# Kernel optimization log

Measured on AMD Instinct MI355X. Metric: run time of the kernel, lower is better.

## Reference

```python
import jax, jax.numpy as jnp
import numpy as np

G, A = 1024, 20          # graphs, atoms per graph
N = G * A                # nodes = 20480
E = G * A * A            # fc edges within each graph = 409600
H = 128                  # hidden_dim
LATENT = 256             # latent_dim
L = 4                    # num_layers
NFREQ = 10
DIS_DIM = NFREQ * 2 * 3  # 60
EDGE_IN = 2 * H + 9 + DIS_DIM  # 325
MAX_ATOMS = 100


def _lin(k, fin, fout):
    return jax.random.normal(k, (fin, fout), dtype=jnp.float32) / np.sqrt(fin).astype(np.float32)


def _stack_lin(k, fin, fout):
    return jnp.stack([_lin(jax.random.fold_in(k, i), fin, fout) for i in range(L)])


def setup_inputs() -> dict:
    key = jax.random.key(0)
    ks = jax.random.split(key, 16)
    atom_types = jax.random.randint(ks[0], (N,), 0, MAX_ATOMS, dtype=jnp.int32)
    frac_coords = jax.random.uniform(ks[1], (N, 3), dtype=jnp.float32)
    lattices = jax.random.normal(ks[2], (G, 3, 3), dtype=jnp.float32)
    t = jax.random.normal(ks[3], (G, LATENT), dtype=jnp.float32)
    # fully-connected (fc) edges within each graph, block-diagonal structure
    base = np.arange(A)
    src = np.repeat(base, A)
    dst = np.tile(base, A)
    offs = (np.arange(G) * A)[:, None]
    edge_index = jnp.asarray(np.stack([
        (src[None, :] + offs).reshape(-1),
        (dst[None, :] + offs).reshape(-1)]), dtype=jnp.int32)  # [2, E]
    edge2graph = jnp.asarray(np.repeat(np.arange(G), A * A), dtype=jnp.int32)
    node2graph = jnp.asarray(np.repeat(np.arange(G), A), dtype=jnp.int32)
    # parameters
    emb_table = jax.random.normal(ks[4], (MAX_ATOMS, H), dtype=jnp.float32) * 0.02
    w_latent = _lin(ks[5], H + LATENT, H)
    b_latent = jnp.zeros((H,), jnp.float32)
    edge_w1 = _stack_lin(ks[6], EDGE_IN, H)
    edge_b1 = jnp.zeros((L, H), jnp.float32)
    edge_w2 = _stack_lin(ks[7], H, H)
    edge_b2 = jnp.zeros((L, H), jnp.float32)
    node_w1 = _stack_lin(ks[8], 2 * H, H)
    node_b1 = jnp.zeros((L, H), jnp.float32)
    node_w2 = _stack_lin(ks[9], H, H)
    node_b2 = jnp.zeros((L, H), jnp.float32)
    coord_w = _lin(ks[10], H, 3)
    lattice_w = _lin(ks[11], H, 9)
    return dict(atom_types=atom_types, frac_coords=frac_coords, lattices=lattices, t=t,
                edge_index=edge_index, edge2graph=edge2graph, node2graph=node2graph,
                emb_table=emb_table, w_latent=w_latent, b_latent=b_latent,
                edge_w1=edge_w1, edge_b1=edge_b1, edge_w2=edge_w2, edge_b2=edge_b2,
                node_w1=node_w1, node_b1=node_b1, node_w2=node_w2, node_b2=node_b2,
                coord_w=coord_w, lattice_w=lattice_w)


def reference(atom_types, frac_coords, lattices, t, edge_index, edge2graph, node2graph,
              emb_table, w_latent, b_latent,
              edge_w1, edge_b1, edge_w2, edge_b2,
              node_w1, node_b1, node_w2, node_b2,
              coord_w, lattice_w):
    silu = jax.nn.silu
    src, dst = edge_index[0], edge_index[1]
    # node embedding + latent conditioning
    h = emb_table[atom_types]                               # [N,H]
    h = jnp.concatenate([h, t[node2graph]], axis=1) @ w_latent + b_latent  # [N,H]
    # sinusoidal distance embedding of periodic frac diff (detached in original)
    frac_diff = (frac_coords[dst] - frac_coords[src]) % 1.0  # [E,3]
    freqs = 2.0 * jnp.pi * jnp.arange(NFREQ, dtype=frac_coords.dtype)
    emb = (frac_diff[..., None] * freqs).reshape(-1, 3 * NFREQ)
    dis = jax.lax.stop_gradient(jnp.concatenate([jnp.sin(emb), jnp.cos(emb)], axis=-1))  # [E,60]
    # lattice inner products, broadcast to edges (ip=True)
    lat_ip = jnp.einsum('gij,gkj->gik', lattices, lattices).reshape(-1, 9)
    lat_edges = lat_ip[edge2graph]                          # [E,9]
    # per-node edge counts for scatter-mean
    counts = jax.ops.segment_sum(jnp.ones_like(src, dtype=h.dtype), src, num_segments=N)
    inv_counts = (1.0 / jnp.maximum(counts, 1.0))[:, None]
    for i in range(L):
        e_in = jnp.concatenate([h[src], h[dst], lat_edges, dis], axis=1)  # [E,325]
        ef = silu(e_in @ edge_w1[i] + edge_b1[i])
        ef = silu(ef @ edge_w2[i] + edge_b2[i])               # [E,H]
        agg = jax.ops.segment_sum(ef, src, num_segments=N) * inv_counts   # scatter-mean
        n_in = jnp.concatenate([h, agg], axis=1)              # [N,2H]
        nf = silu(n_in @ node_w1[i] + node_b1[i])
        nf = silu(nf @ node_w2[i] + node_b2[i])
        h = h + nf                                            # residual
    coord_out = h @ coord_w                                   # [N,3]
    gcounts = jax.ops.segment_sum(jnp.ones((h.shape[0],), h.dtype), node2graph, num_segments=G)
    graph_feat = jax.ops.segment_sum(h, node2graph, num_segments=G) / gcounts[:, None]
    lattice_out = (graph_feat @ lattice_w).reshape(-1, 3, 3)
    lattice_out = jnp.einsum('bij,bjk->bik', lattice_out, lattices)  # ip=True
    return lattice_out, coord_out
```

## Files before the change

kernel.cpp:

```cpp
#include <hip/hip_runtime.h>
#include <stdint.h>


#define NA 20
#define HH 128

typedef unsigned short U16;
typedef unsigned int   U32;
typedef __attribute__((ext_vector_type(8))) short bf8;
typedef __attribute__((ext_vector_type(4))) float f4;

__device__ __forceinline__ float bf2f(U16 u){ return __uint_as_float(((U32)u)<<16); }
__device__ __forceinline__ U16 f2bf(float f){
    return (U16)((__float_as_uint(f) + 0x8000u) >> 16);
}
__device__ __forceinline__ float silu_f(float x){ return x/(1.0f+__expf(-x)); }
template<bool BF>
__device__ __forceinline__ float ldf(const void* p, long i){
    return BF ? bf2f(((const U16*)p)[i]) : ((const float*)p)[i];
}
__device__ __forceinline__ f4 mfma(bf8 a, bf8 b, f4 c){
    return __builtin_amdgcn_mfma_f32_16x16x32_bf16(a,b,c,0,0,0);
}
__device__ __forceinline__ bf8 ldsA(const U16* base, int stride, int row0,
                                    int kbase, int lrow, int quad){
    return *(const bf8*)(base + (row0+lrow)*stride + kbase + quad*8);
}
template<bool BF, bool WS>
__device__ __forceinline__ bf8 getB(const U16* wsb, long wbase, int kt, int nt,
                                    int lane, const void* W, long gbase, int N,
                                    int col, int kbase, int kmax, int quad){
    if constexpr(WS){
        return *(const bf8*)(wsb + wbase + (((long)kt*8 + nt)*64 + lane)*8);
    } else {
        bf8 b; int ks0 = kbase + quad*8;
#pragma unroll
        for(int j=0;j<8;j++){
            int k=ks0+j; U16 v=0;
            if(k<kmax) v = BF ? ((const U16*)W)[gbase+(long)k*N+col]
                              : f2bf(((const float*)W)[gbase+(long)k*N+col]);
            b[j]=(short)v;
        }
        return b;
    }
}

#define WS_LBASE(L) (49152 + (long)(L)*106496)
#define REPACK_BYTES 950272

__global__ __launch_bounds__(256) void repack(
    const void* wlat, const void* ew1, const void* ew2,
    const void* nw1p, const void* nw2p, const void* lat, U16* out)
{
    __shared__ int sG[4];
    const int tid=threadIdx.x;
    {
        const U16* l16=(const U16*)lat; int good=0;
#pragma unroll
        for(int u=0;u<32;u++){
            U16 x=l16[tid*32+u]; int e=(x>>7)&0xFF; good+=(e>=100&&e<=150)?1:0;
        }
#pragma unroll
        for(int o=32;o>0;o>>=1) good+=__shfl_xor(good,o);
        if((tid&63)==0) sG[tid>>6]=good;
    }
    __syncthreads();
    const bool bf = (sG[0]+sG[1]+sG[2]+sG[3]) > 6144;

    const void* W; long srow; int segk; long dst;
    const int ktg=blockIdx.x;
    if(ktg<12){ W=wlat; srow=(long)ktg*32; segk=32; dst=(long)ktg*4096; }
    else{
        int r=ktg-12, L=r/26, lk=r-26*L;
        dst = 49152 + (long)L*106496 + (long)lk*4096;
        if(lk<4)      { W=ew1;  srow=(long)L*325+lk*32;          segk=32; }
        else if(lk<8) { W=ew1;  srow=(long)L*325+128+(lk-4)*32;  segk=32; }
        else if(lk<10){ W=ew1;  srow=(long)L*325+265+(lk-8)*32;  segk=60-(lk-8)*32; }
        else if(lk<14){ W=ew2;  srow=(long)L*128+(lk-10)*32;     segk=32; }
        else if(lk<22){ W=nw1p; srow=(long)L*256+(lk-14)*32;     segk=32; }
        else          { W=nw2p; srow=(long)L*128+(lk-22)*32;     segk=32; }
    }
    for(int o=tid;o<4096;o+=256){
        int nt=o>>9, lane=(o>>3)&63, j=o&7;
        int kk=((lane>>4)<<3)+j, col=nt*16+(lane&15);
        U16 v=0;
        if(kk<segk){
            long idx=(srow+kk)*128+col;
            v = bf ? ((const U16*)W)[idx] : f2bf(((const float*)W)[idx]);
        }
        out[dst+o]=v;
    }
}

#define PB_OFF 8960
#define QB_OFF 11520
#define DB_OFF 14080
#define EB_OFF 19840

template<bool BF, bool WS>
__device__ void body(U16* sm, float* red, const U16* wsb, int g, int tid,
    const int* __restrict__ atype, const void* frac, const void* lattices,
    const void* t, const void* emb, const void* wlat, const void* blat,
    const void* ew1, const void* eb1, const void* ew2, const void* eb2,
    const void* nw1p, const void* nb1, const void* nw2p, const void* nb2,
    const void* coordw, const void* latw, void* outv)
{
    const int lane=tid&63, w=tid>>6, lrow=lane&15, quad=lane>>4;
    const int c = w*16 + lrow;
    U16* HA=sm; U16* pB=sm+PB_OFF; U16* qB=sm+QB_OFF;
    U16* dB=sm+DB_OFF; U16* eB=sm+EB_OFF;
    U16* k1A=eB;
    float* tvecF=(float*)dB;

    for(int q=tid;q<8960;q+=512) HA[q]=0;
    for(int q=tid;q<32*136;q+=512){
        int n=q/136, cc=q-n*136; U16 v=0;
        if(n<20 && cc<128)
            v = BF ? ((const U16*)emb)[(long)atype[g*NA+n]*HH+cc]
                   : f2bf(((const float*)emb)[(long)atype[g*NA+n]*HH+cc]);
        k1A[q]=v;
    }
    {
        int sl=tid>>7, j=tid&127; float acc=0.f;
        for(int kk=0;kk<64;kk++){
            int k=sl*64+kk;
            acc += ldf<BF>(t,(long)g*256+k)*ldf<BF>(wlat,(long)(HH+k)*HH+j);
        }
        tvecF[sl*128+j]=acc;
    }
    __syncthreads();
    {
        f4 a0={0.f,0.f,0.f,0.f}, a1={0.f,0.f,0.f,0.f};
#pragma unroll
        for(int ks=0;ks<4;ks++){
            bf8 b=getB<BF,WS>(wsb,0,ks,w,lane, wlat,0,HH,c,ks*32,128,quad);
            bf8 v0=ldsA(k1A,136,0,ks*32,lrow,quad);
            bf8 v1=ldsA(k1A,136,16,ks*32,lrow,quad);
            a0=mfma(v0,b,a0); a1=mfma(v1,b,a1);
        }
        float bias=ldf<BF>(blat,c)+tvecF[c]+tvecF[128+c]+tvecF[256+c]+tvecF[384+c];
#pragma unroll
        for(int r=0;r<4;r++){
            int r0=quad*4+r, r1=16+quad*4+r;
            if(r0<20) HA[r0*280+c]=f2bf(a0[r]+bias);
            if(r1<20) HA[r1*280+c]=f2bf(a1[r]+bias);
        }
    }
    __syncthreads();
    for(int q=tid;q<80*72;q+=512) dB[q]=0;

    for(int L=0;L<4;L++){
        const long e1=(long)L*325*HH;
        const long LB=WS_LBASE(L);
        if(tid<HH){
            float la[9];
#pragma unroll
            for(int m2=0;m2<9;m2++) la[m2]=ldf<BF>(lattices,(long)g*9+m2);
            float Rv=ldf<BF>(eb1,(long)L*HH+tid);
#pragma unroll
            for(int a2=0;a2<3;a2++)
#pragma unroll
            for(int b3=0;b3<3;b3++){
                float ip=0.f;
#pragma unroll
                for(int c2=0;c2<3;c2++) ip+=la[a2*3+c2]*la[b3*3+c2];
                Rv += ip*ldf<BF>(ew1, e1+(long)(256+a2*3+b3)*HH+tid);
            }
            red[tid]=Rv;
        }
        __syncthreads();
        {
            f4 p0={0.f,0.f,0.f,0.f}, p1={0.f,0.f,0.f,0.f};
#pragma unroll
            for(int ks=0;ks<4;ks++){
                bf8 b=getB<BF,WS>(wsb,LB,ks,w,lane, ew1,e1,HH,c,ks*32,128,quad);
                bf8 v0=ldsA(HA,280,0,ks*32,lrow,quad);
                bf8 v1=ldsA(HA,280,16,ks*32,lrow,quad);
                p0=mfma(v0,b,p0); p1=mfma(v1,b,p1);
            }
            float Rc=red[c];
#pragma unroll
            for(int r=0;r<4;r++){
                int r0=quad*4+r, r1=16+quad*4+r;
                if(r0<20) pB[r0*HH+c]=f2bf(p0[r]+Rc);
                if(r1<20) pB[r1*HH+c]=f2bf(p1[r]+Rc);
            }
        }
        {
            f4 q0={0.f,0.f,0.f,0.f}, q1={0.f,0.f,0.f,0.f};
#pragma unroll
            for(int ks=0;ks<4;ks++){
                bf8 b=getB<BF,WS>(wsb,LB+16384,ks,w,lane, ew1,e1+128*HH,HH,c,ks*32,128,quad);
                bf8 v0=ldsA(HA,280,0,ks*32,lrow,quad);
                bf8 v1=ldsA(HA,280,16,ks*32,lrow,quad);
                q0=mfma(v0,b,q0); q1=mfma(v1,b,q1);
            }
#pragma unroll
            for(int r=0;r<4;r++){
                int r0=quad*4+r, r1=16+quad*4+r;
                if(r0<20) qB[r0*HH+c]=f2bf(q0[r]);
                if(r1<20) qB[r1*HH+c]=f2bf(q1[r]);
            }
        }
        bf8 w1d0=getB<BF,WS>(wsb,LB+32768,0,w,lane, ew1,e1+(long)265*HH,HH,c,0, 60,quad);
        bf8 w1d1=getB<BF,WS>(wsb,LB+32768,1,w,lane, ew1,e1+(long)265*HH,HH,c,32,60,quad);
        bf8 w2f[4];
#pragma unroll
        for(int ks=0;ks<4;ks++)
            w2f[ks]=getB<BF,WS>(wsb,LB+40960,ks,w,lane, ew2,(long)L*HH*HH,HH,c,ks*32,128,quad);
        const float b2=ldf<BF>(eb2,(long)L*HH+c);
        __syncthreads();

        for(int ch=0;ch<5;ch++){
            for(int p=tid;p<2400;p+=512){
                int r=p/30, kk=p-r*30;
                int dim=kk/10, f=kk-dim*10;
                int s=ch*4+(r&3), d=r>>2;
                float fs=ldf<BF>(frac,(long)(g*NA+s)*3+dim);
                float fd=ldf<BF>(frac,(long)(g*NA+d)*3+dim);
                float rev=(float)f*(fd-fs);
                rev=__builtin_amdgcn_fractf(rev);
                dB[r*72+kk]   =f2bf(__builtin_amdgcn_sinf(rev));
                dB[r*72+kk+30]=f2bf(__builtin_amdgcn_cosf(rev));
            }
            __syncthreads();
            float pv[4];
#pragma unroll
            for(int r=0;r<4;r++) pv[r]=bf2f(pB[(ch*4+r)*HH+c]);
#pragma unroll
            for(int m=0;m<5;m++){
                f4 a={0.f,0.f,0.f,0.f};
                bf8 v0=ldsA(dB,72,m*16,0, lrow,quad);
                bf8 v1=ldsA(dB,72,m*16,32,lrow,quad);
                a=mfma(v0,w1d0,a); a=mfma(v1,w1d1,a);
                float qd=bf2f(qB[(m*4+quad)*HH+c]);
#pragma unroll
                for(int r=0;r<4;r++){
                    int row=m*16+quad*4+r;
                    eB[row*136+c]=f2bf(silu_f(a[r]+pv[r]+qd));
                }
            }
            __syncthreads();
            float part[4]={0.f,0.f,0.f,0.f};
#pragma unroll
            for(int m=0;m<5;m++){
                f4 a={0.f,0.f,0.f,0.f};
#pragma unroll
                for(int ks=0;ks<4;ks++){
                    bf8 v=ldsA(eB,136,m*16,ks*32,lrow,quad);
                    a=mfma(v,w2f[ks],a);
                }
#pragma unroll
                for(int r=0;r<4;r++) part[r]+=silu_f(a[r]+b2);
            }
#pragma unroll
            for(int r=0;r<4;r++){
                float v=part[r];
                v+=__shfl_xor(v,16); v+=__shfl_xor(v,32);
                part[r]=v;
            }
            if(quad==0){
#pragma unroll
                for(int r=0;r<4;r++)
                    HA[(ch*4+r)*280+128+c]=f2bf(part[r]*0.05f);
            }
            __syncthreads();
        }
        {
            f4 a0={0.f,0.f,0.f,0.f}, a1={0.f,0.f,0.f,0.f};
#pragma unroll
            for(int ks=0;ks<8;ks++){
                bf8 b=getB<BF,WS>(wsb,LB+57344,ks,w,lane, nw1p,(long)L*256*HH,HH,c,ks*32,256,quad);
                bf8 v0=ldsA(HA,280,0,ks*32,lrow,quad);
                bf8 v1=ldsA(HA,280,16,ks*32,lrow,quad);
                a0=mfma(v0,b,a0); a1=mfma(v1,b,a1);
            }
            float n1=ldf<BF>(nb1,(long)L*HH+c);
#pragma unroll
            for(int r=0;r<4;r++){
                int r0=quad*4+r, r1=16+quad*4+r;
                eB[r0*136+c]=f2bf(r0<20 ? silu_f(a0[r]+n1) : 0.f);
                eB[r1*136+c]=f2bf(r1<20 ? silu_f(a1[r]+n1) : 0.f);
            }
        }
        __syncthreads();
        {
            f4 a0={0.f,0.f,0.f,0.f}, a1={0.f,0.f,0.f,0.f};
#pragma unroll
            for(int ks=0;ks<4;ks++){
                bf8 b=getB<BF,WS>(wsb,LB+90112,ks,w,lane, nw2p,(long)L*HH*HH,HH,c,ks*32,128,quad);
                bf8 v0=ldsA(eB,136,0,ks*32,lrow,quad);
                bf8 v1=ldsA(eB,136,16,ks*32,lrow,quad);
                a0=mfma(v0,b,a0); a1=mfma(v1,b,a1);
            }
            float n2=ldf<BF>(nb2,(long)L*HH+c);
#pragma unroll
            for(int r=0;r<4;r++){
                int r0=quad*4+r, r1=16+quad*4+r;
                if(r0<20) HA[r0*280+c]=f2bf(bf2f(HA[r0*280+c])+silu_f(a0[r]+n2));
                if(r1<20) HA[r1*280+c]=f2bf(bf2f(HA[r1*280+c])+silu_f(a1[r]+n2));
            }
        }
        __syncthreads();
    }

    if(tid<60){
        int n=tid/3, cc=tid-(tid/3)*3; float acc=0.f;
        for(int k=0;k<HH;k++) acc+=bf2f(HA[n*280+k])*ldf<BF>(coordw,(long)k*3+cc);
        if(BF) ((U16*)outv)[(long)1024*9+(long)(g*NA+n)*3+cc]=f2bf(acc);
        else   ((float*)outv)[(long)1024*9+(long)(g*NA+n)*3+cc]=acc;
    }
    if(tid<HH){
        float s2=0.f;
        for(int n=0;n<NA;n++) s2+=bf2f(HA[n*280+tid]);
        red[tid]=s2*0.05f;
    }
    __syncthreads();
    if(tid<9){
        float acc=0.f;
        for(int k=0;k<HH;k++) acc+=red[k]*ldf<BF>(latw,(long)k*9+tid);
        red[HH+tid]=acc;
    }
    __syncthreads();
    if(tid<9){
        int i2=tid/3, k2=tid-(tid/3)*3; float acc=0.f;
#pragma unroll
        for(int j3=0;j3<3;j3++)
            acc+=red[HH+i2*3+j3]*ldf<BF>(lattices,(long)g*9+j3*3+k2);
        if(BF) ((U16*)outv)[(long)g*9+tid]=f2bf(acc);
        else   ((float*)outv)[(long)g*9+tid]=acc;
    }
}

template<bool WS>
__device__ void mega_impl(const U16* wsb,
    const int* atype, const void* frac, const void* lattices, const void* t,
    const void* emb, const void* wlat, const void* blat,
    const void* ew1, const void* eb1, const void* ew2, const void* eb2,
    const void* nw1p, const void* nb1, const void* nw2p, const void* nb2,
    const void* coordw, const void* latw, void* outv)
{
    __shared__ __align__(16) unsigned char smraw[62080];
    U16* sm = (U16*)smraw;
    float* red = (float*)(smraw+61440);
    const int g=blockIdx.x, tid=threadIdx.x, w=tid>>6, lane=tid&63;
    int* di=(int*)red;
    {
        const U16* l16=(const U16*)lattices; int good=0;
#pragma unroll
        for(int u=0;u<16;u++){
            U16 x=l16[tid*16+u]; int e=(x>>7)&0xFF; good+=(e>=100&&e<=150)?1:0;
        }
#pragma unroll
        for(int o=32;o>0;o>>=1) good+=__shfl_xor(good,o);
        if(lane==0) di[w]=good;
    }
    __syncthreads();
    if(tid==0){ int s=0; for(int i=0;i<8;i++) s+=di[i]; di[8]=(s>6144)?1:0; }
    __syncthreads();
    const int bfm=di[8];
    __syncthreads();
    if(bfm) body<true ,WS>(sm,red,wsb,g,tid,atype,frac,lattices,t,emb,wlat,blat,
                           ew1,eb1,ew2,eb2,nw1p,nb1,nw2p,nb2,coordw,latw,outv);
    else    body<false,WS>(sm,red,wsb,g,tid,atype,frac,lattices,t,emb,wlat,blat,
                           ew1,eb1,ew2,eb2,nw1p,nb1,nw2p,nb2,coordw,latw,outv);
}

__global__ __launch_bounds__(512,2) void mega_ws(const U16* wsb,
    const int* atype, const void* frac, const void* lattices, const void* t,
    const void* emb, const void* wlat, const void* blat,
    const void* ew1, const void* eb1, const void* ew2, const void* eb2,
    const void* nw1p, const void* nb1, const void* nw2p, const void* nb2,
    const void* coordw, const void* latw, void* outv)
{
    mega_impl<true>(wsb,atype,frac,lattices,t,emb,wlat,blat,ew1,eb1,ew2,eb2,
                    nw1p,nb1,nw2p,nb2,coordw,latw,outv);
}

__global__ __launch_bounds__(512,2) void mega_direct(const U16* wsb,
    const int* atype, const void* frac, const void* lattices, const void* t,
    const void* emb, const void* wlat, const void* blat,
    const void* ew1, const void* eb1, const void* ew2, const void* eb2,
    const void* nw1p, const void* nb1, const void* nw2p, const void* nb2,
    const void* coordw, const void* latw, void* outv)
{
    mega_impl<false>(wsb,atype,frac,lattices,t,emb,wlat,blat,ew1,eb1,ew2,eb2,
                     nw1p,nb1,nw2p,nb2,coordw,latw,outv);
}

extern "C" void kernel_launch(void* const* d_in, const int* in_sizes, int n_in,
                              void* d_out, int out_size, void* d_ws, size_t ws_size,
                              hipStream_t stream)
{
    (void)in_sizes; (void)n_in; (void)out_size;
    const int* atype = (const int*)d_in[0];
    if(ws_size >= REPACK_BYTES){
        repack<<<116, 256, 0, stream>>>(d_in[8], d_in[10], d_in[12], d_in[14],
                                        d_in[16], d_in[2], (U16*)d_ws);
        mega_ws<<<1024, 512, 0, stream>>>((const U16*)d_ws,
            atype, d_in[1], d_in[2], d_in[3], d_in[7], d_in[8], d_in[9],
            d_in[10], d_in[11], d_in[12], d_in[13], d_in[14], d_in[15],
            d_in[16], d_in[17], d_in[18], d_in[19], d_out);
    } else {
        mega_direct<<<1024, 512, 0, stream>>>(nullptr,
            atype, d_in[1], d_in[2], d_in[3], d_in[7], d_in[8], d_in[9],
            d_in[10], d_in[11], d_in[12], d_in[13], d_in[14], d_in[15],
            d_in[16], d_in[17], d_in[18], d_in[19], d_out);
    }
}
```

Baseline: 437.5 us.

## Precompute per-node sin/cos tables and build edge distance features via angle-difference identities

Per-node sin/cos of f*frac are computed once into a shared table. Edge distance features then come from the sin/cos angle-difference identities instead of transcendentals per edge. Staging of the next chunk's features is moved after the barrier, so one barrier per chunk is removed. The final coord and lattice projections are spread across more threads with shuffle reductions. This adds about 4.8KB of LDS, which could affect occupancy at 2 blocks per CU, and the identity may change rounding slightly versus fract-then-sin.

```diff
diff --git a/kernel.cpp b/kernel.cpp
--- a/kernel.cpp
+++ b/kernel.cpp
@@ -97,8 +97,24 @@
 #define DB_OFF 14080
 #define EB_OFF 19840
 
+__device__ __forceinline__ void stage_dis(U16* dB, const float* tb, int ch, int tid){
+    const float2* t2=(const float2*)tb;
+#pragma unroll
+    for(int it=0; it<5; ++it){
+        int p = tid + it*512;
+        int r = p>>5, j = p&31;
+        if(j<30){
+            int s = ch*4 + (r&3), d = r>>2;
+            float2 vs = t2[s*30+j];
+            float2 vd = t2[d*30+j];
+            dB[r*72+j]    = f2bf(vd.x*vs.y - vd.y*vs.x);
+            dB[r*72+j+30] = f2bf(vd.y*vs.y + vd.x*vs.x);
+        }
+    }
+}
+
 template<bool BF, bool WS>
-__device__ void body(U16* sm, float* red, const U16* wsb, int g, int tid,
+__device__ void body(U16* sm, float* red, float* tb, const U16* wsb, int g, int tid,
     const int* __restrict__ atype, const void* frac, const void* lattices,
     const void* t, const void* emb, const void* wlat, const void* blat,
     const void* ew1, const void* eb1, const void* ew2, const void* eb2,
@@ -120,6 +136,16 @@
                    : f2bf(((const float*)emb)[(long)atype[g*NA+n]*HH+cc]);
         k1A[q]=v;
     }
+    for(int q=tid;q<600;q+=512){
+        int n=q/30, jj=q-n*30;
+        int dim=jj/10, f=jj-dim*10;
+        float x = ldf<BF>(frac,(long)(g*NA+n)*3+dim);
+        float rev = __builtin_amdgcn_fractf((float)f*x);
+        float2 sc;
+        sc.x=__builtin_amdgcn_sinf(rev);
+        sc.y=__builtin_amdgcn_cosf(rev);
+        ((float2*)tb)[q]=sc;
+    }
     {
         int sl=tid>>7, j=tid&127; float acc=0.f;
         for(int kk=0;kk<64;kk++){
@@ -209,21 +235,10 @@
         for(int ks=0;ks<4;ks++)
             w2f[ks]=getB<BF,WS>(wsb,LB+40960,ks,w,lane, ew2,(long)L*HH*HH,HH,c,ks*32,128,quad);
         const float b2=ldf<BF>(eb2,(long)L*HH+c);
+        stage_dis(dB,tb,0,tid);
         __syncthreads();
 
         for(int ch=0;ch<5;ch++){
-            for(int p=tid;p<2400;p+=512){
-                int r=p/30, kk=p-r*30;
-                int dim=kk/10, f=kk-dim*10;
-                int s=ch*4+(r&3), d=r>>2;
-                float fs=ldf<BF>(frac,(long)(g*NA+s)*3+dim);
-                float fd=ldf<BF>(frac,(long)(g*NA+d)*3+dim);
-                float rev=(float)f*(fd-fs);
-                rev=__builtin_amdgcn_fractf(rev);
-                dB[r*72+kk]   =f2bf(__builtin_amdgcn_sinf(rev));
-                dB[r*72+kk+30]=f2bf(__builtin_amdgcn_cosf(rev));
-            }
-            __syncthreads();
             float pv[4];
 #pragma unroll
             for(int r=0;r<4;r++) pv[r]=bf2f(pB[(ch*4+r)*HH+c]);
@@ -241,6 +256,7 @@
                 }
             }
             __syncthreads();
+            if(ch<4) stage_dis(dB,tb,ch+1,tid);
             float part[4]={0.f,0.f,0.f,0.f};
 #pragma unroll
             for(int m=0;m<5;m++){
@@ -304,11 +320,22 @@
         __syncthreads();
     }
 
-    if(tid<60){
-        int n=tid/3, cc=tid-(tid/3)*3; float acc=0.f;
-        for(int k=0;k<HH;k++) acc+=bf2f(HA[n*280+k])*ldf<BF>(coordw,(long)k*3+cc);
-        if(BF) ((U16*)outv)[(long)1024*9+(long)(g*NA+n)*3+cc]=f2bf(acc);
-        else   ((float*)outv)[(long)1024*9+(long)(g*NA+n)*3+cc]=acc;
+    {
+        int o=tid>>3, l8=tid&7;
+        float acc=0.f;
+        int n=o/3, cc=o-n*3;
+        if(o<60){
+#pragma unroll
+            for(int k8=0;k8<16;k8++){
+                int k=l8*16+k8;
+                acc += bf2f(HA[n*280+k]) * ldf<BF>(coordw,(long)k*3+cc);
+            }
+        }
+        acc+=__shfl_xor(acc,1); acc+=__shfl_xor(acc,2); acc+=__shfl_xor(acc,4);
+        if(o<60 && l8==0){
+            if(BF) ((U16*)outv)[(long)1024*9+(long)(g*NA+n)*3+cc]=f2bf(acc);
+            else   ((float*)outv)[(long)1024*9+(long)(g*NA+n)*3+cc]=acc;
+        }
     }
     if(tid<HH){
         float s2=0.f;
@@ -316,10 +343,19 @@
         red[tid]=s2*0.05f;
     }
     __syncthreads();
-    if(tid<9){
+    {
+        int o=tid>>4, l16=tid&15;
         float acc=0.f;
-        for(int k=0;k<HH;k++) acc+=red[k]*ldf<BF>(latw,(long)k*9+tid);
-        red[HH+tid]=acc;
+        if(o<9){
+#pragma unroll
+            for(int k8=0;k8<8;k8++){
+                int k=l16*8+k8;
+                acc += red[k]*ldf<BF>(latw,(long)k*9+o);
+            }
+        }
+        acc+=__shfl_xor(acc,1); acc+=__shfl_xor(acc,2);
+        acc+=__shfl_xor(acc,4); acc+=__shfl_xor(acc,8);
+        if(o<9 && l16==0) red[HH+o]=acc;
     }
     __syncthreads();
     if(tid<9){
@@ -340,9 +376,10 @@
     const void* nw1p, const void* nb1, const void* nw2p, const void* nb2,
     const void* coordw, const void* latw, void* outv)
 {
-    __shared__ __align__(16) unsigned char smraw[62080];
+    __shared__ __align__(16) unsigned char smraw[66880];
     U16* sm = (U16*)smraw;
     float* red = (float*)(smraw+61440);
+    float* tb  = (float*)(smraw+62080);
     const int g=blockIdx.x, tid=threadIdx.x, w=tid>>6, lane=tid&63;
     int* di=(int*)red;
     {
@@ -360,9 +397,9 @@
     __syncthreads();
     const int bfm=di[8];
     __syncthreads();
-    if(bfm) body<true ,WS>(sm,red,wsb,g,tid,atype,frac,lattices,t,emb,wlat,blat,
+    if(bfm) body<true ,WS>(sm,red,tb,wsb,g,tid,atype,frac,lattices,t,emb,wlat,blat,
                            ew1,eb1,ew2,eb2,nw1p,nb1,nw2p,nb2,coordw,latw,outv);
-    else    body<false,WS>(sm,red,wsb,g,tid,atype,frac,lattices,t,emb,wlat,blat,
+    else    body<false,WS>(sm,red,tb,wsb,g,tid,atype,frac,lattices,t,emb,wlat,blat,
                            ew1,eb1,ew2,eb2,nw1p,nb1,nw2p,nb2,coordw,latw,outv);
 }
 
```

Result: faster. 398.3 us (-8.9%).
